# Performance work log

Hardware: AMD Instinct MI355X
Metric: run time of the kernel (lower is better)

The kernel has to match this reference:

```python
import jax, jax.numpy as jnp
import numpy as np

N, M, E, DIM = 100000, 2000, 400000, 128
GIN = 2 * DIM + 3  # gate MLP input width


def _mlp2(x, W1, b1, W2, b2):
    # Linear -> ReLU -> Linear
    return jnp.maximum(x @ W1 + b1, 0.0) @ W2 + b2


def setup_inputs() -> dict:
    key = jax.random.key(0)
    ks = jax.random.split(key, 20)
    s = lambda fan_in: 1.0 / np.sqrt(fan_in)
    inp = {
        "res_feat": jax.random.normal(ks[0], (N, DIM), jnp.float32),
        "meta_feat": jax.random.normal(ks[1], (M, DIM), jnp.float32),
        "sec_ids": jax.random.randint(ks[2], (N,), 0, M),
        "batch_pe_vector": jax.random.normal(ks[3], (N, 3), jnp.float32),
        "batch_meta_2_node_edge": jax.random.randint(ks[4], (2, E), 0, M),
        "batch_meta_2_node_vector": jax.random.normal(ks[5], (E, 3), jnp.float32),
        # gate1 params
        "g1_W1": jax.random.uniform(ks[6], (GIN, DIM), jnp.float32, -s(GIN), s(GIN)),
        "g1_b1": jnp.zeros((DIM,), jnp.float32),
        "g1_W2": jax.random.uniform(ks[7], (DIM, DIM), jnp.float32, -s(DIM), s(DIM)),
        "g1_b2": jnp.zeros((DIM,), jnp.float32),
        # gate2 params
        "g2_W1": jax.random.uniform(ks[8], (GIN, DIM), jnp.float32, -s(GIN), s(GIN)),
        "g2_b1": jnp.zeros((DIM,), jnp.float32),
        "g2_W2": jax.random.uniform(ks[9], (DIM, DIM), jnp.float32, -s(DIM), s(DIM)),
        "g2_b2": jnp.zeros((DIM,), jnp.float32),
        # fuse params
        "f_W1": jax.random.uniform(ks[10], (DIM, DIM), jnp.float32, -s(DIM), s(DIM)),
        "f_b1": jnp.zeros((DIM,), jnp.float32),
        "f_W2": jax.random.uniform(ks[11], (DIM, DIM), jnp.float32, -s(DIM), s(DIM)),
        "f_b2": jnp.zeros((DIM,), jnp.float32),
    }
    return inp


def reference(res_feat, meta_feat, sec_ids, batch_pe_vector,
              batch_meta_2_node_edge, batch_meta_2_node_vector,
              g1_W1, g1_b1, g1_W2, g1_b2,
              g2_W1, g2_b1, g2_W2, g2_b2,
              f_W1, f_b1, f_W2, f_b2):
    n = res_feat.shape[0]
    # gate1: per-node gather of meta features
    meta_broadcast = meta_feat[sec_ids]                       # [N, dim]
    gate1_in = jnp.concatenate([res_feat, meta_broadcast, -batch_pe_vector], axis=-1)
    gate1_w = _mlp2(gate1_in, g1_W1, g1_b1, g1_W2, g1_b2)     # [N, dim]
    # gate2: per-edge gathers
    src, dst = batch_meta_2_node_edge[0], batch_meta_2_node_edge[1]
    meta_add = meta_feat[src]                                 # [E, dim]
    res_b = res_feat[dst]                                     # [E, dim]
    gate2_in = jnp.concatenate([res_b, meta_add, batch_meta_2_node_vector], axis=-1)
    gate2_w = _mlp2(gate2_in, g2_W1, g2_b1, g2_W2, g2_b2)     # [E, dim]
    # scatter_mean over destination nodes
    vals = gate2_w * meta_add
    sums = jax.ops.segment_sum(vals, dst, num_segments=n)
    cnts = jax.ops.segment_sum(jnp.ones((vals.shape[0],), vals.dtype), dst, num_segments=n)
    meta_add_fea = sums / jnp.maximum(cnts, 1.0)[:, None]
    fused = res_feat + gate1_w * meta_broadcast + meta_add_fea
    return _mlp2(fused, f_W1, f_b1, f_W2, f_b2)
```

## Files before the change

### kernel.cpp

```cpp
#include <hip/hip_runtime.h>


typedef short bf16x8 __attribute__((ext_vector_type(8)));
typedef float f32x4  __attribute__((ext_vector_type(4)));

#define XS_PAD 136

__device__ __forceinline__ unsigned short f2bf(float f){
  union { float f; unsigned u; } v; v.f = f;
  return (unsigned short)((v.u + 0x7FFFu + ((v.u >> 16) & 1u)) >> 16);
}
__device__ __forceinline__ unsigned pack2(float a, float b){
  return (unsigned)f2bf(a) | ((unsigned)f2bf(b) << 16);
}

__device__ __forceinline__ void mfma_layer(const unsigned short* Xs,
                                           const bf16x8 (&B)[2][4],
                                           int lane, f32x4 (&acc)[4][2]) {
  const int lcol = lane & 15, quad = lane >> 4;
  #pragma unroll
  for (int rg = 0; rg < 4; ++rg) {
    bf16x8 A[4];
    const unsigned short* ab = Xs + (rg*16 + lcol)*XS_PAD + quad*8;
    #pragma unroll
    for (int kk = 0; kk < 4; ++kk) A[kk] = *(const bf16x8*)(ab + kk*32);
    #pragma unroll
    for (int ctl = 0; ctl < 2; ++ctl)
      #pragma unroll
      for (int kk = 0; kk < 4; ++kk)
        acc[rg][ctl] = __builtin_amdgcn_mfma_f32_16x16x32_bf16(
            A[kk], B[ctl][kk], acc[rg][ctl], 0, 0, 0);
  }
}

__device__ __forceinline__ void load_bfrags(const unsigned short* __restrict__ Wt,
                                            int wave, int lane, bf16x8 (&B)[2][4]) {
  const int lcol = lane & 15, quad = lane >> 4;
  #pragma unroll
  for (int ctl = 0; ctl < 2; ++ctl) {
    int col = (wave*2 + ctl)*16 + lcol;
    #pragma unroll
    for (int kk = 0; kk < 4; ++kk)
      B[ctl][kk] = *(const bf16x8*)(Wt + (size_t)col*128 + kk*32 + quad*8);
  }
}

__device__ __forceinline__ void zero_acc(f32x4 (&acc)[4][2]) {
  #pragma unroll
  for (int rg = 0; rg < 4; ++rg)
    #pragma unroll
    for (int ctl = 0; ctl < 2; ++ctl) {
      acc[rg][ctl][0]=0.f; acc[rg][ctl][1]=0.f;
      acc[rg][ctl][2]=0.f; acc[rg][ctl][3]=0.f;
    }
}

struct WPtrs { const float* s[8]; };
__global__ __launch_bounds__(256) void transpose_w8(WPtrs p,
                                                    unsigned short* __restrict__ dstbase,
                                                    int* __restrict__ counts, int M) {
  int slab = blockIdx.x >> 4, blk = blockIdx.x & 15;
  const float* W = p.s[slab];
  unsigned short* Wt = dstbase + (size_t)slab*16384;
  int c  = blk*8 + (threadIdx.x >> 5);
  int k0 = (threadIdx.x & 31) * 4;
  unsigned short o[4];
  #pragma unroll
  for (int j = 0; j < 4; ++j) o[j] = f2bf(W[(size_t)(k0 + j)*128 + c]);
  *(uint2*)(Wt + (size_t)c*128 + k0) =
      make_uint2((unsigned)o[0] | ((unsigned)o[1] << 16),
                 (unsigned)o[2] | ((unsigned)o[3] << 16));
  int tid = blockIdx.x*256 + threadIdx.x;
  int tot = gridDim.x*256;
  for (int i = tid; i < M; i += tot) counts[i] = 0;
}

__global__ __launch_bounds__(256) void prep_and_hist(
    const float* __restrict__ res, const float* __restrict__ meta,
    const unsigned short* __restrict__ WAt, const unsigned short* __restrict__ WBt,
    const unsigned short* __restrict__ WCt, const float* __restrict__ b1,
    float* __restrict__ A2, float* __restrict__ M2, float* __restrict__ M1,
    int mrows, int nbPrep,
    const int* __restrict__ dst, int* __restrict__ counts, int E) {
  if ((int)blockIdx.x >= nbPrep) {
    int e = ((int)blockIdx.x - nbPrep)*256 + threadIdx.x;
    if (e < E) atomicAdd(&counts[dst[e]], 1);
    return;
  }
  __shared__ __align__(16) unsigned short Xs[64*XS_PAD];
  const int t = threadIdx.x, lane = t & 63, wave = t >> 6;
  const int quad = lane >> 4, lcol = lane & 15;
  const int third = nbPrep / 3;
  const int yy = (int)blockIdx.x / third;
  const int bx = (int)blockIdx.x - yy*third;
  const int tile0 = bx * 64;
  const float* X = (yy == 0) ? res : meta;
  const unsigned short* Wt = (yy == 0) ? WAt : (yy == 1) ? WBt : WCt;
  float* Y = (yy == 0) ? A2 : (yy == 1) ? M2 : M1;
  bf16x8 B[2][4];
  load_bfrags(Wt, wave, lane, B);
  #pragma unroll
  for (int i = 0; i < 8; ++i) {
    int f = t + i*256, row = f >> 5, c4 = f & 31;
    int gr = tile0 + row;
    float4 v = make_float4(0.f,0.f,0.f,0.f);
    if (gr < mrows) v = *(const float4*)(X + (size_t)gr*128 + c4*4);
    *(uint2*)(Xs + row*XS_PAD + c4*4) = make_uint2(pack2(v.x,v.y), pack2(v.z,v.w));
  }
  __syncthreads();
  f32x4 acc[4][2]; zero_acc(acc);
  mfma_layer(Xs, B, lane, acc);
  #pragma unroll
  for (int rg = 0; rg < 4; ++rg)
    #pragma unroll
    for (int ctl = 0; ctl < 2; ++ctl) {
      int col = (wave*2 + ctl)*16 + lcol;
      float badd = 0.f;
      if (yy == 0) badd = b1[col];
      #pragma unroll
      for (int reg = 0; reg < 4; ++reg) {
        int gr = tile0 + rg*16 + quad*4 + reg;
        if (gr < mrows) Y[(size_t)gr*128 + col] = acc[rg][ctl][reg] + badd;
      }
    }
}

__global__ __launch_bounds__(1024) void scan_all(const int* __restrict__ counts,
                                                 int* __restrict__ row_start,
                                                 int* __restrict__ cursor, int M) {
  __shared__ int s[1024];
  __shared__ int carry_s;
  const int t = threadIdx.x;
  if (t == 0) carry_s = 0;
  __syncthreads();
  for (int base = 0; base < M; base += 2048) {
    int i0 = base + 2*t, i1 = i0 + 1;
    int c0 = (i0 < M) ? counts[i0] : 0;
    int c1 = (i1 < M) ? counts[i1] : 0;
    int pair = c0 + c1;
    s[t] = pair; __syncthreads();
    for (int off = 1; off < 1024; off <<= 1) {
      int x = (t >= off) ? s[t-off] : 0; __syncthreads();
      s[t] += x; __syncthreads();
    }
    int carry = carry_s;
    int excl = carry + s[t] - pair;
    if (i0 < M) { row_start[i0] = excl;       cursor[i0] = excl; }
    if (i1 < M) { row_start[i1] = excl + c0;  cursor[i1] = excl + c0; }
    __syncthreads();
    if (t == 1023) carry_s = carry + s[1023];
    __syncthreads();
  }
}

__global__ void fill_kernel(const int* __restrict__ dst, const int* __restrict__ src,
                            const float* __restrict__ evec, int* __restrict__ cursor,
                            float4* __restrict__ edata, int E) {
  int e = blockIdx.x*256 + threadIdx.x;
  if (e < E) {
    int p = atomicAdd(&cursor[dst[e]], 1);
    edata[p] = make_float4(__int_as_float(src[e]),
                           evec[(size_t)e*3], evec[(size_t)e*3+1], evec[(size_t)e*3+2]);
  }
}

__global__ __launch_bounds__(256) void edge_mfma(
    const float* __restrict__ A2, const float* __restrict__ M2,
    const float* __restrict__ meta, const float4* __restrict__ edata,
    const int* __restrict__ row_start, const int* __restrict__ counts,
    const float* __restrict__ g2W1full,
    const unsigned short* __restrict__ W2t, const float* __restrict__ b2,
    float* __restrict__ SUM) {
  const int n = blockIdx.x;
  const int cnt = counts[n];
  if (cnt <= 0) return;
  const int rs = row_start[n];

  __shared__ __align__(16) unsigned short Xh[64*XS_PAD];
  __shared__ int srcl[64];
  __shared__ float evl[192];
  const int t = threadIdx.x, lane = t & 63, wave = t >> 6;
  const int quad = lane >> 4, lcol = lane & 15;
  const int c0 = (t & 31) * 4, rbase = t >> 5;

  float4 ed = make_float4(0.f,0.f,0.f,0.f);
  if (t < 64 && t < cnt) ed = edata[rs + t];

  bf16x8 BW2[2][4];
  load_bfrags(W2t, wave, lane, BW2);
  float4 base = *(const float4*)(A2 + (size_t)n*128 + c0);
  float4 w0 = *(const float4*)(g2W1full + 256*128 + c0);
  float4 w1 = *(const float4*)(g2W1full + 257*128 + c0);
  float4 w2 = *(const float4*)(g2W1full + 258*128 + c0);
  const int colA = wave*32 + lcol, colB = colA + 16;
  const float b2A = b2[colA], b2B = b2[colB];
  float psA = 0.f, psB = 0.f;

  for (int t0 = 0; t0 < cnt; t0 += 64) {
    if (t0) __syncthreads();
    if (t < 64) {
      srcl[t] = __float_as_int(ed.x);
      evl[3*t] = ed.y; evl[3*t+1] = ed.z; evl[3*t+2] = ed.w;
      int idx = t0 + 64 + t;
      ed = make_float4(0.f,0.f,0.f,0.f);
      if (idx < cnt) ed = edata[rs + idx];
    }
    __syncthreads();
    float mvA[16], mvB[16];
    #pragma unroll
    for (int rg = 0; rg < 4; ++rg)
      #pragma unroll
      for (int reg = 0; reg < 4; ++reg) {
        int k = rg*4 + reg, rl = rg*16 + quad*4 + reg;
        int s = srcl[rl];
        mvA[k] = meta[(size_t)s*128 + colA];
        mvB[k] = meta[(size_t)s*128 + colB];
      }
    #pragma unroll
    for (int i = 0; i < 8; ++i) {
      int row = rbase + 8*i;
      float4 h = make_float4(0.f,0.f,0.f,0.f);
      if (t0 + row < cnt) {
        int s = srcl[row];
        float4 m = *(const float4*)(M2 + (size_t)s*128 + c0);
        float e0 = evl[3*row], e1 = evl[3*row+1], e2 = evl[3*row+2];
        h.x = fmaxf(base.x + m.x + e0*w0.x + e1*w1.x + e2*w2.x, 0.f);
        h.y = fmaxf(base.y + m.y + e0*w0.y + e1*w1.y + e2*w2.y, 0.f);
        h.z = fmaxf(base.z + m.z + e0*w0.z + e1*w1.z + e2*w2.z, 0.f);
        h.w = fmaxf(base.w + m.w + e0*w0.w + e1*w1.w + e2*w2.w, 0.f);
      }
      *(uint2*)(Xh + row*XS_PAD + c0) = make_uint2(pack2(h.x,h.y), pack2(h.z,h.w));
    }
    __syncthreads();
    f32x4 acc[4][2]; zero_acc(acc);
    mfma_layer(Xh, BW2, lane, acc);
    #pragma unroll
    for (int rg = 0; rg < 4; ++rg)
      #pragma unroll
      for (int reg = 0; reg < 4; ++reg) {
        int k = rg*4 + reg, rl = rg*16 + quad*4 + reg;
        if (t0 + rl < cnt) {
          psA += (acc[rg][0][reg] + b2A) * mvA[k];
          psB += (acc[rg][1][reg] + b2B) * mvB[k];
        }
      }
  }
  psA += __shfl_xor(psA, 16, 64); psA += __shfl_xor(psA, 32, 64);
  psB += __shfl_xor(psB, 16, 64); psB += __shfl_xor(psB, 32, 64);
  if (quad == 0) {
    SUM[(size_t)n*128 + colA] = psA;
    SUM[(size_t)n*128 + colB] = psB;
  }
}

__global__ __launch_bounds__(256) void fused_node(
    const float* __restrict__ res, const float* __restrict__ meta,
    const int* __restrict__ sec_ids, const float* __restrict__ pe,
    const float* __restrict__ g1W1full, const float* __restrict__ M1,
    const unsigned short* __restrict__ g1At,
    const unsigned short* __restrict__ g1W2t, const float* __restrict__ g1b1,
    const float* __restrict__ g1b2,
    const unsigned short* __restrict__ fW1t, const float* __restrict__ fb1v,
    const unsigned short* __restrict__ fW2t, const float* __restrict__ fb2v,
    const float* __restrict__ SUM, const int* __restrict__ counts, int msize,
    float* __restrict__ out, int rows) {
  __shared__ __align__(16) unsigned short Xs[64*XS_PAD];
  __shared__ int   sids[64];
  __shared__ float pel[192];
  __shared__ float inv[64];
  const int t = threadIdx.x, lane = t & 63, wave = t >> 6;
  const int quad = lane >> 4, lcol = lane & 15;
  const int tile0 = blockIdx.x * 64;
  const int c0 = (t & 31) * 4, rbase = t >> 5;
  const int colA = wave*32 + lcol, colB = colA + 16;

  if (t < 64) {
    int gr = tile0 + t;
    sids[t] = (gr < rows) ? sec_ids[gr] : 0;
    float p0=0.f,p1=0.f,p2=0.f;
    if (gr < rows){ p0=pe[(size_t)gr*3]; p1=pe[(size_t)gr*3+1]; p2=pe[(size_t)gr*3+2]; }
    pel[3*t]=p0; pel[3*t+1]=p1; pel[3*t+2]=p2;
    int c = (gr < rows && gr < msize) ? counts[gr] : 0;
    inv[t] = (c > 0) ? 1.f/(float)c : 0.f;
  }
  bf16x8 BF[2][4];
  load_bfrags(g1At, wave, lane, BF);
  #pragma unroll
  for (int i = 0; i < 8; ++i) {
    int row = rbase + 8*i, gr = tile0 + row;
    float4 v = make_float4(0.f,0.f,0.f,0.f);
    if (gr < rows) v = *(const float4*)(res + (size_t)gr*128 + c0);
    *(uint2*)(Xs + row*XS_PAD + c0) = make_uint2(pack2(v.x,v.y), pack2(v.z,v.w));
  }
  __syncthreads();
  f32x4 acc[4][2]; zero_acc(acc);
  mfma_layer(Xs, BF, lane, acc);
  load_bfrags(g1W2t, wave, lane, BF);
  __syncthreads();
  {
    const float b1A = g1b1[colA], b1B = g1b1[colB];
    const float wA0 = g1W1full[256*128+colA], wA1 = g1W1full[257*128+colA],
                wA2 = g1W1full[258*128+colA];
    const float wB0 = g1W1full[256*128+colB], wB1 = g1W1full[257*128+colB],
                wB2 = g1W1full[258*128+colB];
    #pragma unroll
    for (int rg = 0; rg < 4; ++rg)
      #pragma unroll
      for (int reg = 0; reg < 4; ++reg) {
        int row = rg*16 + quad*4 + reg;
        int sid = sids[row];
        float m1A = M1[(size_t)sid*128 + colA];
        float m1B = M1[(size_t)sid*128 + colB];
        float p0 = pel[3*row], p1 = pel[3*row+1], p2 = pel[3*row+2];
        float vA = acc[rg][0][reg] + m1A + b1A - p0*wA0 - p1*wA1 - p2*wA2;
        float vB = acc[rg][1][reg] + m1B + b1B - p0*wB0 - p1*wB1 - p2*wB2;
        Xs[row*XS_PAD + colA] = f2bf(fmaxf(vA, 0.f));
        Xs[row*XS_PAD + colB] = f2bf(fmaxf(vB, 0.f));
      }
  }
  __syncthreads();
  zero_acc(acc);
  mfma_layer(Xs, BF, lane, acc);
  load_bfrags(fW1t, wave, lane, BF);
  __syncthreads();
  {
    const float b2A = g1b2[colA], b2B = g1b2[colB];
    #pragma unroll
    for (int rg = 0; rg < 4; ++rg)
      #pragma unroll
      for (int reg = 0; reg < 4; ++reg) {
        int row = rg*16 + quad*4 + reg, gr = tile0 + row;
        unsigned short oA = 0, oB = 0;
        if (gr < rows) {
          int sid = sids[row];
          float gA = acc[rg][0][reg] + b2A, gB = acc[rg][1][reg] + b2B;
          float mA = meta[(size_t)sid*128 + colA], mB = meta[(size_t)sid*128 + colB];
          float rA = res[(size_t)gr*128 + colA],  rB = res[(size_t)gr*128 + colB];
          float iv = inv[row];
          float sA = 0.f, sB = 0.f;
          if (iv > 0.f) {
            sA = SUM[(size_t)gr*128 + colA] * iv;
            sB = SUM[(size_t)gr*128 + colB] * iv;
          }
          oA = f2bf(rA + gA*mA + sA);
          oB = f2bf(rB + gB*mB + sB);
        }
        Xs[row*XS_PAD + colA] = oA;
        Xs[row*XS_PAD + colB] = oB;
      }
  }
  __syncthreads();
  zero_acc(acc);
  mfma_layer(Xs, BF, lane, acc);
  load_bfrags(fW2t, wave, lane, BF);
  __syncthreads();
  {
    const float fb1A = fb1v[colA], fb1B = fb1v[colB];
    #pragma unroll
    for (int rg = 0; rg < 4; ++rg)
      #pragma unroll
      for (int reg = 0; reg < 4; ++reg) {
        int row = rg*16 + quad*4 + reg;
        Xs[row*XS_PAD + colA] = f2bf(fmaxf(acc[rg][0][reg] + fb1A, 0.f));
        Xs[row*XS_PAD + colB] = f2bf(fmaxf(acc[rg][1][reg] + fb1B, 0.f));
      }
  }
  __syncthreads();
  zero_acc(acc);
  mfma_layer(Xs, BF, lane, acc);
  {
    const float fb2A = fb2v[colA], fb2B = fb2v[colB];
    #pragma unroll
    for (int rg = 0; rg < 4; ++rg)
      #pragma unroll
      for (int reg = 0; reg < 4; ++reg) {
        int gr = tile0 + rg*16 + quad*4 + reg;
        if (gr < rows) {
          out[(size_t)gr*128 + colA] = acc[rg][0][reg] + fb2A;
          out[(size_t)gr*128 + colB] = acc[rg][1][reg] + fb2B;
        }
      }
  }
}

extern "C" void kernel_launch(void* const* d_in, const int* in_sizes, int n_in,
                              void* d_out, int out_size, void* d_ws, size_t ws_size,
                              hipStream_t stream) {
  const float* res     = (const float*)d_in[0];
  const float* meta    = (const float*)d_in[1];
  const int*   sec_ids = (const int*)  d_in[2];
  const float* pe      = (const float*)d_in[3];
  const int*   edge    = (const int*)  d_in[4];
  const float* evec    = (const float*)d_in[5];
  const float* g1W1 = (const float*)d_in[6];
  const float* g1b1 = (const float*)d_in[7];
  const float* g1W2 = (const float*)d_in[8];
  const float* g1b2 = (const float*)d_in[9];
  const float* g2W1 = (const float*)d_in[10];
  const float* g2b1 = (const float*)d_in[11];
  const float* g2W2 = (const float*)d_in[12];
  const float* g2b2 = (const float*)d_in[13];
  const float* fW1  = (const float*)d_in[14];
  const float* fb1  = (const float*)d_in[15];
  const float* fW2  = (const float*)d_in[16];
  const float* fb2  = (const float*)d_in[17];

  const int N = in_sizes[0] / 128;
  const int M = in_sizes[1] / 128;
  const int E = in_sizes[4] / 2;
  const int* src = edge;
  const int* dst = edge + E;

  float* ws = (float*)d_ws;
  float* A2   = ws;
  float* M2   = A2 + (size_t)M*128;
  float* M1   = M2 + (size_t)M*128;
  float* SUMb = M1 + (size_t)M*128;
  int* counts     = (int*)(SUMb + (size_t)M*128);
  int* row_startp = counts + M;
  int* cursor     = row_startp + M;
  uintptr_t ap = (uintptr_t)(cursor + M);
  ap = (ap + 15) & ~(uintptr_t)15;
  float4* edata = (float4*)ap;
  uintptr_t wp = (uintptr_t)(edata + E);
  wp = (wp + 15) & ~(uintptr_t)15;
  unsigned short* Wt = (unsigned short*)wp;
  unsigned short* W_g1A  = Wt + 0*16384;
  unsigned short* W_g1B  = Wt + 1*16384;
  unsigned short* W_g1W2 = Wt + 2*16384;
  unsigned short* W_g2A  = Wt + 3*16384;
  unsigned short* W_g2B  = Wt + 4*16384;
  unsigned short* W_g2W2 = Wt + 5*16384;
  unsigned short* W_fW1  = Wt + 6*16384;
  unsigned short* W_fW2  = Wt + 7*16384;
  float* out = (float*)d_out;

  WPtrs p;
  p.s[0] = g1W1;            p.s[1] = g1W1 + 128*128;  p.s[2] = g1W2;
  p.s[3] = g2W1;            p.s[4] = g2W1 + 128*128;  p.s[5] = g2W2;
  p.s[6] = fW1;             p.s[7] = fW2;

  const int nbMt   = (M + 63) / 64;
  const int nbN    = (N + 63) / 64;
  const int nbE    = (E + 255) / 256;
  const int nbPrep = 3*nbMt;

  transpose_w8<<<128, 256, 0, stream>>>(p, Wt, counts, M);
  prep_and_hist<<<nbPrep + nbE, 256, 0, stream>>>(res, meta, W_g2A, W_g2B, W_g1B,
                                                  g2b1, A2, M2, M1, M, nbPrep,
                                                  dst, counts, E);
  scan_all<<<1, 1024, 0, stream>>>(counts, row_startp, cursor, M);
  fill_kernel<<<nbE, 256, 0, stream>>>(dst, src, evec, cursor, edata, E);
  edge_mfma<<<M, 256, 0, stream>>>(A2, M2, meta, edata, row_startp, counts,
                                   g2W1, W_g2W2, g2b2, SUMb);
  fused_node<<<nbN, 256, 0, stream>>>(res, meta, sec_ids, pe, g1W1, M1,
                                      W_g1A, W_g1W2, g1b1, g1b2,
                                      W_fW1, fb1, W_fW2, fb2,
                                      SUMb, counts, M, out, N);
}
```

Measured before the change: 368.1 us.

## Process two 64-row tiles per block in fused node kernel

The fused node MLP kernel now handles 128 rows per block as two 64-row sub-tiles with separate shared buffers and accumulators. Each weight fragment loaded into registers is reused across both sub-tiles, halving weight fragment loads and barriers per row. The cost is doubled accumulator registers and shared memory per block, with a launch bound of 4 blocks, which may reduce occupancy or cause spills.

New measurement: 354.4 us. 3.7% less time.

```diff
diff --git a/kernel.cpp b/kernel.cpp
--- a/kernel.cpp
+++ b/kernel.cpp
@@ -253,7 +253,7 @@
   }
 }
 
-__global__ __launch_bounds__(256) void fused_node(
+__global__ __launch_bounds__(256, 4) void fused_node2(
     const float* __restrict__ res, const float* __restrict__ meta,
     const int* __restrict__ sec_ids, const float* __restrict__ pe,
     const float* __restrict__ g1W1full, const float* __restrict__ M1,
@@ -264,18 +264,19 @@
     const unsigned short* __restrict__ fW2t, const float* __restrict__ fb2v,
     const float* __restrict__ SUM, const int* __restrict__ counts, int msize,
     float* __restrict__ out, int rows) {
-  __shared__ __align__(16) unsigned short Xs[64*XS_PAD];
-  __shared__ int   sids[64];
-  __shared__ float pel[192];
-  __shared__ float inv[64];
+  __shared__ __align__(16) unsigned short XsA[64*XS_PAD];
+  __shared__ __align__(16) unsigned short XsB[64*XS_PAD];
+  __shared__ int   sids[128];
+  __shared__ float pel[384];
+  __shared__ float inv[128];
   const int t = threadIdx.x, lane = t & 63, wave = t >> 6;
   const int quad = lane >> 4, lcol = lane & 15;
-  const int tile0 = blockIdx.x * 64;
+  const int base = blockIdx.x * 128;
   const int c0 = (t & 31) * 4, rbase = t >> 5;
   const int colA = wave*32 + lcol, colB = colA + 16;
 
-  if (t < 64) {
-    int gr = tile0 + t;
+  if (t < 128) {
+    int gr = base + t;
     sids[t] = (gr < rows) ? sec_ids[gr] : 0;
     float p0=0.f,p1=0.f,p2=0.f;
     if (gr < rows){ p0=pe[(size_t)gr*3]; p1=pe[(size_t)gr*3+1]; p2=pe[(size_t)gr*3+2]; }
@@ -287,14 +288,23 @@
   load_bfrags(g1At, wave, lane, BF);
   #pragma unroll
   for (int i = 0; i < 8; ++i) {
-    int row = rbase + 8*i, gr = tile0 + row;
+    int row = rbase + 8*i, gr = base + row;
     float4 v = make_float4(0.f,0.f,0.f,0.f);
     if (gr < rows) v = *(const float4*)(res + (size_t)gr*128 + c0);
-    *(uint2*)(Xs + row*XS_PAD + c0) = make_uint2(pack2(v.x,v.y), pack2(v.z,v.w));
-  }
-  __syncthreads();
-  f32x4 acc[4][2]; zero_acc(acc);
-  mfma_layer(Xs, BF, lane, acc);
+    *(uint2*)(XsA + row*XS_PAD + c0) = make_uint2(pack2(v.x,v.y), pack2(v.z,v.w));
+  }
+  #pragma unroll
+  for (int i = 0; i < 8; ++i) {
+    int row = rbase + 8*i, gr = base + 64 + row;
+    float4 v = make_float4(0.f,0.f,0.f,0.f);
+    if (gr < rows) v = *(const float4*)(res + (size_t)gr*128 + c0);
+    *(uint2*)(XsB + row*XS_PAD + c0) = make_uint2(pack2(v.x,v.y), pack2(v.z,v.w));
+  }
+  __syncthreads();
+  f32x4 accA[4][2], accB[4][2];
+  zero_acc(accA); zero_acc(accB);
+  mfma_layer(XsA, BF, lane, accA);
+  mfma_layer(XsB, BF, lane, accB);
   load_bfrags(g1W2t, wave, lane, BF);
   __syncthreads();
   {
@@ -312,15 +322,30 @@
         float m1A = M1[(size_t)sid*128 + colA];
         float m1B = M1[(size_t)sid*128 + colB];
         float p0 = pel[3*row], p1 = pel[3*row+1], p2 = pel[3*row+2];
-        float vA = acc[rg][0][reg] + m1A + b1A - p0*wA0 - p1*wA1 - p2*wA2;
-        float vB = acc[rg][1][reg] + m1B + b1B - p0*wB0 - p1*wB1 - p2*wB2;
-        Xs[row*XS_PAD + colA] = f2bf(fmaxf(vA, 0.f));
-        Xs[row*XS_PAD + colB] = f2bf(fmaxf(vB, 0.f));
-      }
-  }
-  __syncthreads();
-  zero_acc(acc);
-  mfma_layer(Xs, BF, lane, acc);
+        float vA = accA[rg][0][reg] + m1A + b1A - p0*wA0 - p1*wA1 - p2*wA2;
+        float vB = accA[rg][1][reg] + m1B + b1B - p0*wB0 - p1*wB1 - p2*wB2;
+        XsA[row*XS_PAD + colA] = f2bf(fmaxf(vA, 0.f));
+        XsA[row*XS_PAD + colB] = f2bf(fmaxf(vB, 0.f));
+      }
+    #pragma unroll
+    for (int rg = 0; rg < 4; ++rg)
+      #pragma unroll
+      for (int reg = 0; reg < 4; ++reg) {
+        int row = rg*16 + quad*4 + reg, rr = 64 + row;
+        int sid = sids[rr];
+        float m1A = M1[(size_t)sid*128 + colA];
+        float m1B = M1[(size_t)sid*128 + colB];
+        float p0 = pel[3*rr], p1 = pel[3*rr+1], p2 = pel[3*rr+2];
+        float vA = accB[rg][0][reg] + m1A + b1A - p0*wA0 - p1*wA1 - p2*wA2;
+        float vB = accB[rg][1][reg] + m1B + b1B - p0*wB0 - p1*wB1 - p2*wB2;
+        XsB[row*XS_PAD + colA] = f2bf(fmaxf(vA, 0.f));
+        XsB[row*XS_PAD + colB] = f2bf(fmaxf(vB, 0.f));
+      }
+  }
+  __syncthreads();
+  zero_acc(accA); zero_acc(accB);
+  mfma_layer(XsA, BF, lane, accA);
+  mfma_layer(XsB, BF, lane, accB);
   load_bfrags(fW1t, wave, lane, BF);
   __syncthreads();
   {
@@ -329,11 +354,11 @@
     for (int rg = 0; rg < 4; ++rg)
       #pragma unroll
       for (int reg = 0; reg < 4; ++reg) {
-        int row = rg*16 + quad*4 + reg, gr = tile0 + row;
+        int row = rg*16 + quad*4 + reg, gr = base + row;
         unsigned short oA = 0, oB = 0;
         if (gr < rows) {
           int sid = sids[row];
-          float gA = acc[rg][0][reg] + b2A, gB = acc[rg][1][reg] + b2B;
+          float gA = accA[rg][0][reg] + b2A, gB = accA[rg][1][reg] + b2B;
           float mA = meta[(size_t)sid*128 + colA], mB = meta[(size_t)sid*128 + colB];
           float rA = res[(size_t)gr*128 + colA],  rB = res[(size_t)gr*128 + colB];
           float iv = inv[row];
@@ -345,13 +370,37 @@
           oA = f2bf(rA + gA*mA + sA);
           oB = f2bf(rB + gB*mB + sB);
         }
-        Xs[row*XS_PAD + colA] = oA;
-        Xs[row*XS_PAD + colB] = oB;
-      }
-  }
-  __syncthreads();
-  zero_acc(acc);
-  mfma_layer(Xs, BF, lane, acc);
+        XsA[row*XS_PAD + colA] = oA;
+        XsA[row*XS_PAD + colB] = oB;
+      }
+    #pragma unroll
+    for (int rg = 0; rg < 4; ++rg)
+      #pragma unroll
+      for (int reg = 0; reg < 4; ++reg) {
+        int row = rg*16 + quad*4 + reg, rr = 64 + row, gr = base + rr;
+        unsigned short oA = 0, oB = 0;
+        if (gr < rows) {
+          int sid = sids[rr];
+          float gA = accB[rg][0][reg] + b2A, gB = accB[rg][1][reg] + b2B;
+          float mA = meta[(size_t)sid*128 + colA], mB = meta[(size_t)sid*128 + colB];
+          float rA = res[(size_t)gr*128 + colA],  rB = res[(size_t)gr*128 + colB];
+          float iv = inv[rr];
+          float sA = 0.f, sB = 0.f;
+          if (iv > 0.f) {
+            sA = SUM[(size_t)gr*128 + colA] * iv;
+            sB = SUM[(size_t)gr*128 + colB] * iv;
+          }
+          oA = f2bf(rA + gA*mA + sA);
+          oB = f2bf(rB + gB*mB + sB);
+        }
+        XsB[row*XS_PAD + colA] = oA;
+        XsB[row*XS_PAD + colB] = oB;
+      }
+  }
+  __syncthreads();
+  zero_acc(accA); zero_acc(accB);
+  mfma_layer(XsA, BF, lane, accA);
+  mfma_layer(XsB, BF, lane, accB);
   load_bfrags(fW2t, wave, lane, BF);
   __syncthreads();
   {
@@ -361,23 +410,31 @@
       #pragma unroll
       for (int reg = 0; reg < 4; ++reg) {
         int row = rg*16 + quad*4 + reg;
-        Xs[row*XS_PAD + colA] = f2bf(fmaxf(acc[rg][0][reg] + fb1A, 0.f));
-        Xs[row*XS_PAD + colB] = f2bf(fmaxf(acc[rg][1][reg] + fb1B, 0.f));
-      }
-  }
-  __syncthreads();
-  zero_acc(acc);
-  mfma_layer(Xs, BF, lane, acc);
+        XsA[row*XS_PAD + colA] = f2bf(fmaxf(accA[rg][0][reg] + fb1A, 0.f));
+        XsA[row*XS_PAD + colB] = f2bf(fmaxf(accA[rg][1][reg] + fb1B, 0.f));
+        XsB[row*XS_PAD + colA] = f2bf(fmaxf(accB[rg][0][reg] + fb1A, 0.f));
+        XsB[row*XS_PAD + colB] = f2bf(fmaxf(accB[rg][1][reg] + fb1B, 0.f));
+      }
+  }
+  __syncthreads();
+  zero_acc(accA); zero_acc(accB);
+  mfma_layer(XsA, BF, lane, accA);
+  mfma_layer(XsB, BF, lane, accB);
   {
     const float fb2A = fb2v[colA], fb2B = fb2v[colB];
     #pragma unroll
     for (int rg = 0; rg < 4; ++rg)
       #pragma unroll
       for (int reg = 0; reg < 4; ++reg) {
-        int gr = tile0 + rg*16 + quad*4 + reg;
-        if (gr < rows) {
-          out[(size_t)gr*128 + colA] = acc[rg][0][reg] + fb2A;
-          out[(size_t)gr*128 + colB] = acc[rg][1][reg] + fb2B;
+        int row = rg*16 + quad*4 + reg;
+        int grA = base + row, grB = base + 64 + row;
+        if (grA < rows) {
+          out[(size_t)grA*128 + colA] = accA[rg][0][reg] + fb2A;
+          out[(size_t)grA*128 + colB] = accA[rg][1][reg] + fb2B;
+        }
+        if (grB < rows) {
+          out[(size_t)grB*128 + colA] = accB[rg][0][reg] + fb2A;
+          out[(size_t)grB*128 + colB] = accB[rg][1][reg] + fb2B;
         }
       }
   }
@@ -442,6 +499,7 @@
 
   const int nbMt   = (M + 63) / 64;
   const int nbN    = (N + 63) / 64;
+  const int nbN2   = (nbN + 1) / 2;
   const int nbE    = (E + 255) / 256;
   const int nbPrep = 3*nbMt;
 
@@ -453,8 +511,8 @@
   fill_kernel<<<nbE, 256, 0, stream>>>(dst, src, evec, cursor, edata, E);
   edge_mfma<<<M, 256, 0, stream>>>(A2, M2, meta, edata, row_startp, counts,
                                    g2W1, W_g2W2, g2b2, SUMb);
-  fused_node<<<nbN, 256, 0, stream>>>(res, meta, sec_ids, pe, g1W1, M1,
-                                      W_g1A, W_g1W2, g1b1, g1b2,
-                                      W_fW1, fb1, W_fW2, fb2,
-                                      SUMb, counts, M, out, N);
-}
+  fused_node2<<<nbN2, 256, 0, stream>>>(res, meta, sec_ids, pe, g1W1, M1,
+                                        W_g1A, W_g1W2, g1b1, g1b2,
+                                        W_fW1, fb1, W_fW2, fb2,
+                                        SUMb, counts, M, out, N);
+}
```
